# Optimization experiments

Measured on AMD Instinct MI355X. Metric: run time of the kernel, lower is better.

Reference implementation:

```python
import jax, jax.numpy as jnp
import numpy as np

N_NODES = 100000
N_EDGES = 3200000
IN_CH = 256


def setup_inputs() -> dict:
    key = jax.random.key(0)
    ks = jax.random.split(key, 8)
    x = jax.random.normal(ks[0], (N_NODES, IN_CH), dtype=jnp.float32)
    edge_index = jax.random.randint(ks[1], (2, N_EDGES), 0, N_NODES, dtype=jnp.int64)
    alpha = jnp.ones((), dtype=jnp.float32)
    beta = jnp.ones((), dtype=jnp.float32)
    s = 1.0 / np.sqrt(IN_CH)
    W_mlp = jax.random.normal(ks[2], (1, IN_CH), dtype=jnp.float32) * s
    W_lin = jax.random.normal(ks[3], (1, IN_CH), dtype=jnp.float32) * s
    W_gcn = jax.random.normal(ks[4], (1, IN_CH), dtype=jnp.float32) * s
    W_att = jax.random.normal(ks[5], (3, 3), dtype=jnp.float32) * (1.0 / np.sqrt(3))
    b_att = jax.random.normal(ks[6], (3,), dtype=jnp.float32) * 0.1
    return {"x": x, "edge_index": edge_index, "alpha": alpha, "beta": beta,
            "W_mlp": W_mlp, "W_lin": W_lin, "W_gcn": W_gcn,
            "W_att": W_att, "b_att": b_att}


def _gcn_conv(x, edge_index, W_gcn, num_nodes):
    # PyG GCNConv: add self-loops, symmetric normalization, no bias.
    loop = jnp.arange(num_nodes, dtype=edge_index.dtype)
    row = jnp.concatenate([edge_index[0], loop])  # source
    col = jnp.concatenate([edge_index[1], loop])  # target
    deg = jax.ops.segment_sum(jnp.ones_like(col, dtype=x.dtype), col,
                              num_segments=num_nodes)
    dinv = jnp.where(deg > 0, jax.lax.rsqrt(deg), 0.0)
    norm = dinv[row] * dinv[col]                  # [E+N]
    xw = x @ W_gcn.T                               # [N, 1]
    msg = norm[:, None] * xw[row]                  # [E+N, 1]
    return jax.ops.segment_sum(msg, col, num_segments=num_nodes)  # [N, 1]


def reference(x, edge_index, alpha, beta, W_mlp, W_lin, W_gcn, W_att, b_att):
    num_nodes = x.shape[0]
    # score1: in-degree based
    deg = jax.ops.segment_sum(jnp.ones((edge_index.shape[1],), dtype=x.dtype),
                              edge_index[1], num_segments=num_nodes)
    score1 = jax.nn.sigmoid(alpha * jnp.sqrt(deg) + beta)           # [N]
    # score2: tiny MLP
    score2 = jax.nn.sigmoid((x @ W_mlp.T)[:, 0])                    # [N]
    # score3: GCNConv + linear
    gcn_out = _gcn_conv(x, edge_index, W_gcn, num_nodes)            # [N,1]
    score3 = jax.nn.sigmoid((gcn_out + x @ W_lin.T)[:, 0])          # [N]
    scores = jnp.stack([score1, score2, score3], axis=1)            # [N,3]
    weight = jax.nn.softmax(scores @ W_att.T + b_att, axis=1)       # [N,3]
    fitness = jnp.sum(weight * scores, axis=1)                      # [N]
    return fitness
```

## Files before the change

### kernel.cpp

```cpp
#include <hip/hip_runtime.h>
#include <math.h>

#define N_CH    256
#define SBSHIFT 11
#define SBN     2048
#define NSMAX   64
#define CH      4096

__device__ __forceinline__ float sigmoidf_(float v) {
    return 1.0f / (1.0f + expf(-v));
}

__device__ __forceinline__ void build_tables(const int* sbT, int ns,
                                             int* sbsL, int* cstL) {
    if (threadIdx.x == 0) {
        int run = 0, c = 0;
        for (int i = 0; i < ns; ++i) {
            sbsL[i] = run;
            cstL[i] = c;
            int len = sbT[i];
            run += len;
            c += (len + CH - 1) / CH;
        }
        sbsL[ns] = run;
        cstL[ns] = c;
    }
}

__global__ __launch_bounds__(256) void dots_hist_kernel(
    const float* __restrict__ x,
    const float* __restrict__ Wmlp, const float* __restrict__ Wlin,
    const float* __restrict__ Wgcn, const int* __restrict__ dst,
    float* __restrict__ s2dot, float* __restrict__ s3lin, float* __restrict__ xw,
    int* __restrict__ H1,
    int n_nodes, int n_edges, int ns, int nch)
{
    __shared__ int h[NSMAX];
    if ((int)blockIdx.x < nch) {
        int c = blockIdx.x;
        if (threadIdx.x < NSMAX) h[threadIdx.x] = 0;
        __syncthreads();
        int start = c * CH;
        #pragma unroll
        for (int m = 0; m < 4; ++m) {
            int e = start + (m * 256 + (int)threadIdx.x) * 4;
            if (e + 3 < n_edges) {
                int4 d4 = *(const int4*)(dst + e);
                atomicAdd(&h[d4.x >> SBSHIFT], 1);
                atomicAdd(&h[d4.y >> SBSHIFT], 1);
                atomicAdd(&h[d4.z >> SBSHIFT], 1);
                atomicAdd(&h[d4.w >> SBSHIFT], 1);
            } else {
                for (int ee = e; ee < n_edges && ee >= 0; ++ee)
                    atomicAdd(&h[dst[ee] >> SBSHIFT], 1);
            }
        }
        __syncthreads();
        if (threadIdx.x < (unsigned)ns)
            H1[(size_t)threadIdx.x * nch + c] = h[threadIdx.x];
        return;
    }

    int wid  = ((int)blockIdx.x - nch) * 4 + ((int)threadIdx.x >> 6);
    int lane = threadIdx.x & 63;
    if (wid >= n_nodes) return;

    const float4* xr = (const float4*)(x + (size_t)wid * N_CH);
    float4 v  = xr[lane];
    float4 wm = ((const float4*)Wmlp)[lane];
    float4 wl = ((const float4*)Wlin)[lane];
    float4 wg = ((const float4*)Wgcn)[lane];

    float d0 = v.x*wm.x + v.y*wm.y + v.z*wm.z + v.w*wm.w;
    float d1 = v.x*wl.x + v.y*wl.y + v.z*wl.z + v.w*wl.w;
    float d2 = v.x*wg.x + v.y*wg.y + v.z*wg.z + v.w*wg.w;

    #pragma unroll
    for (int off = 32; off; off >>= 1) {
        d0 += __shfl_down(d0, off, 64);
        d1 += __shfl_down(d1, off, 64);
        d2 += __shfl_down(d2, off, 64);
    }
    if (lane == 0) { s2dot[wid] = d0; s3lin[wid] = d1; xw[wid] = d2; }
}

__global__ __launch_bounds__(1024) void scanA_kernel(
    const int* __restrict__ H1, int* __restrict__ O, int* __restrict__ sbT,
    int nch)
{
    __shared__ int s[1024];
    int sb = blockIdx.x, t = threadIdx.x;
    int v = (t < nch) ? H1[(size_t)sb * nch + t] : 0;
    s[t] = v;
    __syncthreads();
    for (int off = 1; off < 1024; off <<= 1) {
        int a = s[t];
        int b = (t >= off) ? s[t - off] : 0;
        __syncthreads();
        s[t] = a + b;
        __syncthreads();
    }
    if (t < nch) O[(size_t)sb * nch + t] = s[t] - v;
    if (t == 1023) sbT[sb] = s[1023];
}

__global__ __launch_bounds__(256) void scatter_kernel(
    const int* __restrict__ src, const int* __restrict__ dst,
    const int* __restrict__ sbT, const int* __restrict__ O,
    int* __restrict__ cpack, int n_edges, int ns, int nch)
{
    __shared__ int sbsL[NSMAX + 1], cstL[NSMAX + 1];
    __shared__ int pos0[NSMAX];
    __shared__ int lp[NSMAX + 1];
    __shared__ int h[NSMAX];
    __shared__ int sorted[CH];

    int c = blockIdx.x;
    build_tables(sbT, ns, sbsL, cstL);
    if (threadIdx.x < NSMAX) h[threadIdx.x] = 0;
    __syncthreads();
    if (threadIdx.x < (unsigned)ns)
        pos0[threadIdx.x] = sbsL[threadIdx.x] + O[(size_t)threadIdx.x * nch + c];

    int start = c * CH;
    int cnt = n_edges - start; if (cnt > CH) cnt = CH;

    int4 s4[4], d4[4];
    #pragma unroll
    for (int m = 0; m < 4; ++m) {
        int e = start + (m * 256 + (int)threadIdx.x) * 4;
        if (e + 3 < n_edges) {
            s4[m] = *(const int4*)(src + e);
            d4[m] = *(const int4*)(dst + e);
            atomicAdd(&h[d4[m].x >> SBSHIFT], 1);
            atomicAdd(&h[d4[m].y >> SBSHIFT], 1);
            atomicAdd(&h[d4[m].z >> SBSHIFT], 1);
            atomicAdd(&h[d4[m].w >> SBSHIFT], 1);
        } else {
            s4[m] = make_int4(-1, -1, -1, -1);
            int* sp = (int*)&s4[m]; int* dp = (int*)&d4[m];
            for (int j = 0; j < 4; ++j) {
                int ee = e + j;
                if (ee < n_edges && ee >= 0) {
                    sp[j] = src[ee]; dp[j] = dst[ee];
                    atomicAdd(&h[dp[j] >> SBSHIFT], 1);
                }
            }
        }
    }
    __syncthreads();
    if (threadIdx.x == 0) {
        int run = 0;
        for (int i = 0; i < ns; ++i) { lp[i] = run; run += h[i]; }
        lp[ns] = run;
    }
    __syncthreads();
    if (threadIdx.x < NSMAX) h[threadIdx.x] = 0;
    __syncthreads();
    #pragma unroll
    for (int m = 0; m < 4; ++m) {
        int* sp = (int*)&s4[m]; int* dp = (int*)&d4[m];
        #pragma unroll
        for (int j = 0; j < 4; ++j) {
            if (sp[j] >= 0) {
                int d = dp[j];
                int sb = d >> SBSHIFT;
                int r = atomicAdd(&h[sb], 1);
                sorted[lp[sb] + r] = sp[j] | ((d & (SBN - 1)) << 17);
            }
        }
    }
    __syncthreads();
    for (int p = threadIdx.x; p < cnt; p += 256) {
        int lo = 0, hi = ns;
        while (hi - lo > 1) { int mid = (lo + hi) >> 1; if (lp[mid] <= p) lo = mid; else hi = mid; }
        cpack[pos0[lo] + (p - lp[lo])] = sorted[p];
    }
}

__global__ __launch_bounds__(256) void chunkDeg_kernel(
    const int* __restrict__ cpack, const int* __restrict__ sbT,
    int* __restrict__ partialD, int ns)
{
    __shared__ int sbsL[NSMAX + 1], cstL[NSMAX + 1];
    __shared__ int cnt[SBN];
    build_tables(sbT, ns, sbsL, cstL);
    for (int i = threadIdx.x; i < SBN; i += 256) cnt[i] = 0;
    __syncthreads();
    int c = blockIdx.x;
    if (c >= cstL[ns]) return;
    int lo = 0, hi = ns;
    while (hi - lo > 1) { int mid = (lo + hi) >> 1; if (cstL[mid] <= c) lo = mid; else hi = mid; }
    int sb = lo;
    int i0 = c - cstL[sb];
    int base = sbsL[sb] + i0 * CH;
    int len = sbsL[sb + 1] - base; if (len > CH) len = CH;

    #pragma unroll
    for (int m = 0; m < 4; ++m) {
        int e = (m * 256 + (int)threadIdx.x) * 4;
        if (e + 3 < len) {
            int4 w4 = *(const int4*)(cpack + base + e);
            atomicAdd(&cnt[w4.x >> 17], 1);
            atomicAdd(&cnt[w4.y >> 17], 1);
            atomicAdd(&cnt[w4.z >> 17], 1);
            atomicAdd(&cnt[w4.w >> 17], 1);
        } else {
            for (int ee = e; ee < len && ee >= 0; ++ee)
                atomicAdd(&cnt[cpack[base + ee] >> 17], 1);
        }
    }
    __syncthreads();
    int* row = partialD + (size_t)c * SBN;
    for (int i = threadIdx.x; i < SBN; i += 256) row[i] = cnt[i];
}

__global__ __launch_bounds__(256) void reduceDeg_kernel(
    const int* __restrict__ partialD, const int* __restrict__ sbT,
    const float* __restrict__ xw,
    float* __restrict__ degf, float* __restrict__ dinv, float* __restrict__ sxw,
    int n_nodes, int ns)
{
    __shared__ int sbsL[NSMAX + 1], cstL[NSMAX + 1];
    build_tables(sbT, ns, sbsL, cstL);
    __syncthreads();
    int i = blockIdx.x * 256 + threadIdx.x;
    if (i >= n_nodes) return;
    int sb = i >> SBSHIFT, li = i & (SBN - 1);
    int c0 = cstL[sb], c1 = cstL[sb + 1];
    int d = 0;
    for (int c = c0; c < c1; ++c) d += partialD[(size_t)c * SBN + li];
    float df = (float)d;
    degf[i] = df;
    float di = rsqrtf(df + 1.0f);
    dinv[i] = di;
    sxw[i]  = di * xw[i];
}

__global__ __launch_bounds__(256) void chunkAcc_kernel(
    const int* __restrict__ cpack, const int* __restrict__ sbT,
    const float* __restrict__ sxw, float* __restrict__ partialF, int ns)
{
    __shared__ int sbsL[NSMAX + 1], cstL[NSMAX + 1];
    __shared__ float facc[SBN];
    build_tables(sbT, ns, sbsL, cstL);
    for (int i = threadIdx.x; i < SBN; i += 256) facc[i] = 0.0f;
    __syncthreads();
    int c = blockIdx.x;
    if (c >= cstL[ns]) return;
    int lo = 0, hi = ns;
    while (hi - lo > 1) { int mid = (lo + hi) >> 1; if (cstL[mid] <= c) lo = mid; else hi = mid; }
    int sb = lo;
    int i0 = c - cstL[sb];
    int base = sbsL[sb] + i0 * CH;
    int len = sbsL[sb + 1] - base; if (len > CH) len = CH;

    #pragma unroll
    for (int m = 0; m < 4; ++m) {
        int e = (m * 256 + (int)threadIdx.x) * 4;
        if (e + 3 < len) {
            int4 w4 = *(const int4*)(cpack + base + e);
            atomicAdd(&facc[w4.x >> 17], sxw[w4.x & 0x1FFFF]);
            atomicAdd(&facc[w4.y >> 17], sxw[w4.y & 0x1FFFF]);
            atomicAdd(&facc[w4.z >> 17], sxw[w4.z & 0x1FFFF]);
            atomicAdd(&facc[w4.w >> 17], sxw[w4.w & 0x1FFFF]);
        } else {
            for (int ee = e; ee < len && ee >= 0; ++ee) {
                int w = cpack[base + ee];
                atomicAdd(&facc[w >> 17], sxw[w & 0x1FFFF]);
            }
        }
    }
    __syncthreads();
    float* row = partialF + (size_t)c * SBN;
    for (int i = threadIdx.x; i < SBN; i += 256) row[i] = facc[i];
}

__global__ __launch_bounds__(256) void reduceFinal_kernel(
    const float* __restrict__ partialF, const int* __restrict__ sbT,
    const float* __restrict__ degf, const float* __restrict__ dinv,
    const float* __restrict__ xw, const float* __restrict__ s2dot,
    const float* __restrict__ s3lin,
    const float* __restrict__ alpha, const float* __restrict__ beta,
    const float* __restrict__ Watt, const float* __restrict__ batt,
    float* __restrict__ out, int n_nodes, int ns)
{
    __shared__ int sbsL[NSMAX + 1], cstL[NSMAX + 1];
    build_tables(sbT, ns, sbsL, cstL);
    __syncthreads();
    int i = blockIdx.x * 256 + threadIdx.x;
    if (i >= n_nodes) return;
    int sb = i >> SBSHIFT, li = i & (SBN - 1);
    int c0 = cstL[sb], c1 = cstL[sb + 1];
    float acc = 0.0f;
    for (int c = c0; c < c1; ++c) acc += partialF[(size_t)c * SBN + li];

    float dn = dinv[i];
    float g  = acc * dn + dn * dn * xw[i];
    float s1 = sigmoidf_(alpha[0] * sqrtf(degf[i]) + beta[0]);
    float s2 = sigmoidf_(s2dot[i]);
    float s3 = sigmoidf_(g + s3lin[i]);

    float z0 = Watt[0]*s1 + Watt[1]*s2 + Watt[2]*s3 + batt[0];
    float z1 = Watt[3]*s1 + Watt[4]*s2 + Watt[5]*s3 + batt[1];
    float z2 = Watt[6]*s1 + Watt[7]*s2 + Watt[8]*s3 + batt[2];

    float m  = fmaxf(z0, fmaxf(z1, z2));
    float e0 = expf(z0 - m), e1 = expf(z1 - m), e2 = expf(z2 - m);
    float inv = 1.0f / (e0 + e1 + e2);
    out[i] = (e0 * s1 + e1 * s2 + e2 * s3) * inv;
}

extern "C" void kernel_launch(void* const* d_in, const int* in_sizes, int n_in,
                              void* d_out, int out_size, void* d_ws, size_t ws_size,
                              hipStream_t stream) {
    const float* x     = (const float*)d_in[0];
    const int*   ei    = (const int*)d_in[1];
    const float* alpha = (const float*)d_in[2];
    const float* beta  = (const float*)d_in[3];
    const float* Wmlp  = (const float*)d_in[4];
    const float* Wlin  = (const float*)d_in[5];
    const float* Wgcn  = (const float*)d_in[6];
    const float* Watt  = (const float*)d_in[7];
    const float* batt  = (const float*)d_in[8];
    float* out = (float*)d_out;

    int n_nodes = in_sizes[0] / N_CH;
    int n_edges = in_sizes[1] / 2;
    const int* src = ei;
    const int* dst = ei + n_edges;

    int ns  = (n_nodes + SBN - 1) >> SBSHIFT;
    int nch = (n_edges + CH - 1) / CH;
    int maxChunks = nch + ns;

    size_t off = 0;
    int*   cpack    = (int*)d_ws;          off += (((size_t)n_edges + 1023) & ~(size_t)1023);
    int*   H1       = (int*)d_ws + off;    off += (((size_t)ns * nch + 1023) & ~(size_t)1023);
    int*   O        = (int*)d_ws + off;    off += (((size_t)ns * nch + 1023) & ~(size_t)1023);
    int*   sbT      = (int*)d_ws + off;    off += 128;
    int*   partialD = (int*)d_ws + off;    off += (size_t)maxChunks * SBN;
    float* partialF = (float*)d_ws + off;  off += (size_t)maxChunks * SBN;
    float* s2dot    = (float*)d_ws + off;  off += (((size_t)n_nodes + 1023) & ~(size_t)1023);
    float* s3lin    = (float*)d_ws + off;  off += (((size_t)n_nodes + 1023) & ~(size_t)1023);
    float* xw       = (float*)d_ws + off;  off += (((size_t)n_nodes + 1023) & ~(size_t)1023);
    float* degf     = (float*)d_ws + off;  off += (((size_t)n_nodes + 1023) & ~(size_t)1023);
    float* dinv     = (float*)d_ws + off;  off += (((size_t)n_nodes + 1023) & ~(size_t)1023);
    float* sxw      = (float*)d_ws + off;  off += (((size_t)n_nodes + 1023) & ~(size_t)1023);

    int dotsBlocks = (n_nodes + 3) / 4;
    dots_hist_kernel<<<nch + dotsBlocks, 256, 0, stream>>>(
        x, Wmlp, Wlin, Wgcn, dst, s2dot, s3lin, xw, H1,
        n_nodes, n_edges, ns, nch);

    scanA_kernel<<<ns, 1024, 0, stream>>>(H1, O, sbT, nch);

    scatter_kernel<<<nch, 256, 0, stream>>>(src, dst, sbT, O, cpack,
                                            n_edges, ns, nch);

    chunkDeg_kernel<<<maxChunks, 256, 0, stream>>>(cpack, sbT, partialD, ns);

    reduceDeg_kernel<<<(n_nodes + 255) / 256, 256, 0, stream>>>(
        partialD, sbT, xw, degf, dinv, sxw, n_nodes, ns);

    chunkAcc_kernel<<<maxChunks, 256, 0, stream>>>(cpack, sbT, sxw, partialF, ns);

    reduceFinal_kernel<<<(n_nodes + 255) / 256, 256, 0, stream>>>(
        partialF, sbT, degf, dinv, xw, s2dot, s3lin,
        alpha, beta, Watt, batt, out, n_nodes, ns);
}
```

Before: 243.6 us.

## Compute degree with global atomics and merge scatter with degree normalisation

In-degree is now accumulated with global atomics during the histogram pass, which removes the chunkDeg and reduceDeg kernels and their partialD buffer. The degree normalisation runs as extra blocks inside the scatter kernel. The scatter kernel reuses the H1 counts, so its first shared histogram pass goes away. It replaces the serial thread-0 prefix loops with wave shuffle scans and the per-element binary search with a shared lookup table. The histogram is split into 8 copies per bucket to reduce LDS atomic contention. In exchange it adds 3.2M scattered global atomics and a memset.

```diff
diff --git a/kernel.cpp b/kernel.cpp
--- a/kernel.cpp
+++ b/kernel.cpp
@@ -32,32 +32,44 @@
     const float* __restrict__ Wmlp, const float* __restrict__ Wlin,
     const float* __restrict__ Wgcn, const int* __restrict__ dst,
     float* __restrict__ s2dot, float* __restrict__ s3lin, float* __restrict__ xw,
-    int* __restrict__ H1,
+    int* __restrict__ H1, int* __restrict__ deg,
     int n_nodes, int n_edges, int ns, int nch)
 {
-    __shared__ int h[NSMAX];
+    __shared__ int h8[NSMAX * 8];
     if ((int)blockIdx.x < nch) {
         int c = blockIdx.x;
-        if (threadIdx.x < NSMAX) h[threadIdx.x] = 0;
+        for (int i = threadIdx.x; i < NSMAX * 8; i += 256) h8[i] = 0;
         __syncthreads();
+        int copy = (int)threadIdx.x & 7;
         int start = c * CH;
         #pragma unroll
         for (int m = 0; m < 4; ++m) {
             int e = start + (m * 256 + (int)threadIdx.x) * 4;
             if (e + 3 < n_edges) {
                 int4 d4 = *(const int4*)(dst + e);
-                atomicAdd(&h[d4.x >> SBSHIFT], 1);
-                atomicAdd(&h[d4.y >> SBSHIFT], 1);
-                atomicAdd(&h[d4.z >> SBSHIFT], 1);
-                atomicAdd(&h[d4.w >> SBSHIFT], 1);
+                atomicAdd(&h8[(d4.x >> SBSHIFT) * 8 + copy], 1);
+                atomicAdd(&h8[(d4.y >> SBSHIFT) * 8 + copy], 1);
+                atomicAdd(&h8[(d4.z >> SBSHIFT) * 8 + copy], 1);
+                atomicAdd(&h8[(d4.w >> SBSHIFT) * 8 + copy], 1);
+                atomicAdd(&deg[d4.x], 1);
+                atomicAdd(&deg[d4.y], 1);
+                atomicAdd(&deg[d4.z], 1);
+                atomicAdd(&deg[d4.w], 1);
             } else {
-                for (int ee = e; ee < n_edges && ee >= 0; ++ee)
-                    atomicAdd(&h[dst[ee] >> SBSHIFT], 1);
+                for (int ee = e; ee < n_edges && ee >= 0; ++ee) {
+                    int d = dst[ee];
+                    atomicAdd(&h8[(d >> SBSHIFT) * 8 + copy], 1);
+                    atomicAdd(&deg[d], 1);
+                }
             }
         }
         __syncthreads();
-        if (threadIdx.x < (unsigned)ns)
-            H1[(size_t)threadIdx.x * nch + c] = h[threadIdx.x];
+        if (threadIdx.x < (unsigned)ns) {
+            int s = 0;
+            #pragma unroll
+            for (int k = 0; k < 8; ++k) s += h8[threadIdx.x * 8 + k];
+            H1[(size_t)threadIdx.x * nch + c] = s;
+        }
         return;
     }
 
@@ -104,137 +116,95 @@
     if (t == 1023) sbT[sb] = s[1023];
 }
 
-__global__ __launch_bounds__(256) void scatter_kernel(
+__global__ __launch_bounds__(256) void scatter_deg_kernel(
     const int* __restrict__ src, const int* __restrict__ dst,
     const int* __restrict__ sbT, const int* __restrict__ O,
-    int* __restrict__ cpack, int n_edges, int ns, int nch)
-{
-    __shared__ int sbsL[NSMAX + 1], cstL[NSMAX + 1];
-    __shared__ int pos0[NSMAX];
+    const int* __restrict__ H1,
+    const int* __restrict__ deg, const float* __restrict__ xw,
+    float* __restrict__ degf, float* __restrict__ dinv, float* __restrict__ sxw,
+    int* __restrict__ cpack, int n_nodes, int n_edges, int ns, int nch)
+{
+    if ((int)blockIdx.x >= nch) {
+        int i = ((int)blockIdx.x - nch) * 256 + (int)threadIdx.x;
+        if (i < n_nodes) {
+            float df = (float)deg[i];
+            degf[i] = df;
+            float di = rsqrtf(df + 1.0f);
+            dinv[i] = di;
+            sxw[i]  = di * xw[i];
+        }
+        return;
+    }
+
     __shared__ int lp[NSMAX + 1];
-    __shared__ int h[NSMAX];
+    __shared__ int dl[NSMAX];
+    __shared__ int h2[NSMAX];
+    __shared__ unsigned short sbOf[CH];
     __shared__ int sorted[CH];
 
     int c = blockIdx.x;
-    build_tables(sbT, ns, sbsL, cstL);
-    if (threadIdx.x < NSMAX) h[threadIdx.x] = 0;
-    __syncthreads();
-    if (threadIdx.x < (unsigned)ns)
-        pos0[threadIdx.x] = sbsL[threadIdx.x] + O[(size_t)threadIdx.x * nch + c];
+    int t = threadIdx.x;
+
+    if (t < 64) {
+        h2[t] = 0;
+        int hv = (t < ns) ? H1[(size_t)t * nch + c] : 0;
+        int sv = (t < ns) ? sbT[t] : 0;
+        int hi = hv, si = sv;
+        #pragma unroll
+        for (int off = 1; off < 64; off <<= 1) {
+            int a = __shfl_up(hi, off, 64); if (t >= off) hi += a;
+            int b = __shfl_up(si, off, 64); if (t >= off) si += b;
+        }
+        if (t < ns) {
+            int lpe = hi - hv;
+            lp[t] = lpe;
+            int sbs = si - sv;
+            dl[t] = sbs + O[(size_t)t * nch + c] - lpe;
+        }
+        if (t == ns - 1) lp[ns] = hi;
+    }
+    __syncthreads();
+
+    if (t < ns) {
+        int p0 = lp[t], p1 = lp[t + 1];
+        for (int p = p0; p < p1; ++p) sbOf[p] = (unsigned short)t;
+    }
 
     int start = c * CH;
     int cnt = n_edges - start; if (cnt > CH) cnt = CH;
 
-    int4 s4[4], d4[4];
     #pragma unroll
     for (int m = 0; m < 4; ++m) {
-        int e = start + (m * 256 + (int)threadIdx.x) * 4;
+        int e = start + (m * 256 + t) * 4;
         if (e + 3 < n_edges) {
-            s4[m] = *(const int4*)(src + e);
-            d4[m] = *(const int4*)(dst + e);
-            atomicAdd(&h[d4[m].x >> SBSHIFT], 1);
-            atomicAdd(&h[d4[m].y >> SBSHIFT], 1);
-            atomicAdd(&h[d4[m].z >> SBSHIFT], 1);
-            atomicAdd(&h[d4[m].w >> SBSHIFT], 1);
+            int4 s4 = *(const int4*)(src + e);
+            int4 d4 = *(const int4*)(dst + e);
+            int sb, r;
+            sb = d4.x >> SBSHIFT; r = atomicAdd(&h2[sb], 1);
+            sorted[lp[sb] + r] = s4.x | ((d4.x & (SBN - 1)) << 17);
+            sb = d4.y >> SBSHIFT; r = atomicAdd(&h2[sb], 1);
+            sorted[lp[sb] + r] = s4.y | ((d4.y & (SBN - 1)) << 17);
+            sb = d4.z >> SBSHIFT; r = atomicAdd(&h2[sb], 1);
+            sorted[lp[sb] + r] = s4.z | ((d4.z & (SBN - 1)) << 17);
+            sb = d4.w >> SBSHIFT; r = atomicAdd(&h2[sb], 1);
+            sorted[lp[sb] + r] = s4.w | ((d4.w & (SBN - 1)) << 17);
         } else {
-            s4[m] = make_int4(-1, -1, -1, -1);
-            int* sp = (int*)&s4[m]; int* dp = (int*)&d4[m];
             for (int j = 0; j < 4; ++j) {
                 int ee = e + j;
                 if (ee < n_edges && ee >= 0) {
-                    sp[j] = src[ee]; dp[j] = dst[ee];
-                    atomicAdd(&h[dp[j] >> SBSHIFT], 1);
+                    int sv = src[ee], dv = dst[ee];
+                    int sb = dv >> SBSHIFT;
+                    int r = atomicAdd(&h2[sb], 1);
+                    sorted[lp[sb] + r] = sv | ((dv & (SBN - 1)) << 17);
                 }
             }
         }
     }
     __syncthreads();
-    if (threadIdx.x == 0) {
-        int run = 0;
-        for (int i = 0; i < ns; ++i) { lp[i] = run; run += h[i]; }
-        lp[ns] = run;
-    }
-    __syncthreads();
-    if (threadIdx.x < NSMAX) h[threadIdx.x] = 0;
-    __syncthreads();
-    #pragma unroll
-    for (int m = 0; m < 4; ++m) {
-        int* sp = (int*)&s4[m]; int* dp = (int*)&d4[m];
-        #pragma unroll
-        for (int j = 0; j < 4; ++j) {
-            if (sp[j] >= 0) {
-                int d = dp[j];
-                int sb = d >> SBSHIFT;
-                int r = atomicAdd(&h[sb], 1);
-                sorted[lp[sb] + r] = sp[j] | ((d & (SBN - 1)) << 17);
-            }
-        }
-    }
-    __syncthreads();
-    for (int p = threadIdx.x; p < cnt; p += 256) {
-        int lo = 0, hi = ns;
-        while (hi - lo > 1) { int mid = (lo + hi) >> 1; if (lp[mid] <= p) lo = mid; else hi = mid; }
-        cpack[pos0[lo] + (p - lp[lo])] = sorted[p];
-    }
-}
-
-__global__ __launch_bounds__(256) void chunkDeg_kernel(
-    const int* __restrict__ cpack, const int* __restrict__ sbT,
-    int* __restrict__ partialD, int ns)
-{
-    __shared__ int sbsL[NSMAX + 1], cstL[NSMAX + 1];
-    __shared__ int cnt[SBN];
-    build_tables(sbT, ns, sbsL, cstL);
-    for (int i = threadIdx.x; i < SBN; i += 256) cnt[i] = 0;
-    __syncthreads();
-    int c = blockIdx.x;
-    if (c >= cstL[ns]) return;
-    int lo = 0, hi = ns;
-    while (hi - lo > 1) { int mid = (lo + hi) >> 1; if (cstL[mid] <= c) lo = mid; else hi = mid; }
-    int sb = lo;
-    int i0 = c - cstL[sb];
-    int base = sbsL[sb] + i0 * CH;
-    int len = sbsL[sb + 1] - base; if (len > CH) len = CH;
-
-    #pragma unroll
-    for (int m = 0; m < 4; ++m) {
-        int e = (m * 256 + (int)threadIdx.x) * 4;
-        if (e + 3 < len) {
-            int4 w4 = *(const int4*)(cpack + base + e);
-            atomicAdd(&cnt[w4.x >> 17], 1);
-            atomicAdd(&cnt[w4.y >> 17], 1);
-            atomicAdd(&cnt[w4.z >> 17], 1);
-            atomicAdd(&cnt[w4.w >> 17], 1);
-        } else {
-            for (int ee = e; ee < len && ee >= 0; ++ee)
-                atomicAdd(&cnt[cpack[base + ee] >> 17], 1);
-        }
-    }
-    __syncthreads();
-    int* row = partialD + (size_t)c * SBN;
-    for (int i = threadIdx.x; i < SBN; i += 256) row[i] = cnt[i];
-}
-
-__global__ __launch_bounds__(256) void reduceDeg_kernel(
-    const int* __restrict__ partialD, const int* __restrict__ sbT,
-    const float* __restrict__ xw,
-    float* __restrict__ degf, float* __restrict__ dinv, float* __restrict__ sxw,
-    int n_nodes, int ns)
-{
-    __shared__ int sbsL[NSMAX + 1], cstL[NSMAX + 1];
-    build_tables(sbT, ns, sbsL, cstL);
-    __syncthreads();
-    int i = blockIdx.x * 256 + threadIdx.x;
-    if (i >= n_nodes) return;
-    int sb = i >> SBSHIFT, li = i & (SBN - 1);
-    int c0 = cstL[sb], c1 = cstL[sb + 1];
-    int d = 0;
-    for (int c = c0; c < c1; ++c) d += partialD[(size_t)c * SBN + li];
-    float df = (float)d;
-    degf[i] = df;
-    float di = rsqrtf(df + 1.0f);
-    dinv[i] = di;
-    sxw[i]  = di * xw[i];
+
+    for (int p = t; p < cnt; p += 256) {
+        cpack[dl[sbOf[p]] + p] = sorted[p];
+    }
 }
 
 __global__ __launch_bounds__(256) void chunkAcc_kernel(
@@ -339,7 +309,7 @@
     int*   H1       = (int*)d_ws + off;    off += (((size_t)ns * nch + 1023) & ~(size_t)1023);
     int*   O        = (int*)d_ws + off;    off += (((size_t)ns * nch + 1023) & ~(size_t)1023);
     int*   sbT      = (int*)d_ws + off;    off += 128;
-    int*   partialD = (int*)d_ws + off;    off += (size_t)maxChunks * SBN;
+    int*   deg      = (int*)d_ws + off;    off += (((size_t)n_nodes + 1023) & ~(size_t)1023);
     float* partialF = (float*)d_ws + off;  off += (size_t)maxChunks * SBN;
     float* s2dot    = (float*)d_ws + off;  off += (((size_t)n_nodes + 1023) & ~(size_t)1023);
     float* s3lin    = (float*)d_ws + off;  off += (((size_t)n_nodes + 1023) & ~(size_t)1023);
@@ -348,20 +318,19 @@
     float* dinv     = (float*)d_ws + off;  off += (((size_t)n_nodes + 1023) & ~(size_t)1023);
     float* sxw      = (float*)d_ws + off;  off += (((size_t)n_nodes + 1023) & ~(size_t)1023);
 
+    hipMemsetAsync(deg, 0, (size_t)n_nodes * sizeof(int), stream);
+
     int dotsBlocks = (n_nodes + 3) / 4;
     dots_hist_kernel<<<nch + dotsBlocks, 256, 0, stream>>>(
-        x, Wmlp, Wlin, Wgcn, dst, s2dot, s3lin, xw, H1,
+        x, Wmlp, Wlin, Wgcn, dst, s2dot, s3lin, xw, H1, deg,
         n_nodes, n_edges, ns, nch);
 
     scanA_kernel<<<ns, 1024, 0, stream>>>(H1, O, sbT, nch);
 
-    scatter_kernel<<<nch, 256, 0, stream>>>(src, dst, sbT, O, cpack,
-                                            n_edges, ns, nch);
-
-    chunkDeg_kernel<<<maxChunks, 256, 0, stream>>>(cpack, sbT, partialD, ns);
-
-    reduceDeg_kernel<<<(n_nodes + 255) / 256, 256, 0, stream>>>(
-        partialD, sbT, xw, degf, dinv, sxw, n_nodes, ns);
+    int degBlocks = (n_nodes + 255) / 256;
+    scatter_deg_kernel<<<nch + degBlocks, 256, 0, stream>>>(
+        src, dst, sbT, O, H1, deg, xw, degf, dinv, sxw, cpack,
+        n_nodes, n_edges, ns, nch);
 
     chunkAcc_kernel<<<maxChunks, 256, 0, stream>>>(cpack, sbT, sxw, partialF, ns);
 
```

New measurement: 341.8 us. 40.3% more time.
